# Kernel tuning notes

Measured on AMD Instinct MI355X. Metric: run time of the kernel, lower is better.

Reference implementation:

```python
import jax, jax.numpy as jnp
import numpy as np

G = 8          # GroupNorm groups
EPS = 1e-5
L = 4          # num_layers
C = 64         # hidden_channels
CIN = 2        # in_channels


def group_norm(x, gamma, beta):
    B, Cc, H, W = x.shape
    xr = x.reshape(B, G, Cc // G, H, W)
    mu = xr.mean(axis=(2, 3, 4), keepdims=True)
    var = xr.var(axis=(2, 3, 4), keepdims=True)
    xn = ((xr - mu) * jax.lax.rsqrt(var + EPS)).reshape(B, Cc, H, W)
    return xn * gamma[:, None, None] + beta[:, None, None]


def conv1x1(x, w, b):
    # x: [B,Ci,H,W], w: [Co,Ci] -> [B,Co,H,W]
    return jnp.einsum('bchw,oc->bohw', x, w) + b[None, :, None, None]


def conv3x3(x, w, b):
    y = jax.lax.conv_general_dilated(x, w, (1, 1), 'SAME',
                                     dimension_numbers=('NCHW', 'OIHW', 'NCHW'))
    return y + b[None, :, None, None]


def setup_inputs() -> dict:
    key = jax.random.key(0)
    ks = jax.random.split(key, 20)
    s = 0.05
    inp = {
        'x': jax.random.normal(ks[0], (2, CIN, 256, 256), jnp.float32),
        'hidden': jnp.zeros((2, L, C, C), jnp.float32),
        'W_in': jax.random.normal(ks[1], (C, CIN, 3, 3), jnp.float32) * s,
        'b_in': jnp.zeros((C,), jnp.float32),
        'gamma': jnp.ones((L, C), jnp.float32),
        'beta': jnp.zeros((L, C), jnp.float32),
        'Wq': jax.random.normal(ks[2], (L, C, C), jnp.float32) * s,
        'bq': jnp.zeros((L, C), jnp.float32),
        'Wk': jax.random.normal(ks[3], (L, C, C), jnp.float32) * s,
        'bk': jnp.zeros((L, C), jnp.float32),
        'Wv': jax.random.normal(ks[4], (L, C, C), jnp.float32) * s,
        'bv': jnp.zeros((L, C), jnp.float32),
        'Wg': jax.random.normal(ks[5], (L, 2 * C, C), jnp.float32) * s,
        'bg': jnp.zeros((L, 2 * C), jnp.float32),
        'Wp': jax.random.normal(ks[6], (L, C, C), jnp.float32) * s,
        'bp': jnp.zeros((L, C), jnp.float32),
        'W_out': jax.random.normal(ks[7], (CIN, C, 3, 3), jnp.float32) * s,
        'b_out': jnp.zeros((CIN,), jnp.float32),
    }
    return inp


def gla_layer(feat, prev_mem, gamma, beta, Wq, bq, Wk, bk, Wv, bv, Wg, bg, Wp, bp):
    B, Cc, H, W = feat.shape
    N = H * W
    scale = Cc ** (-0.5)
    xn = group_norm(feat, gamma, beta)
    q = conv1x1(xn, Wq, bq).reshape(B, Cc, N) * scale
    k = conv1x1(xn, Wk, bk).reshape(B, Cc, N)
    v = conv1x1(xn, Wv, bv).reshape(B, Cc, N)
    gates = conv1x1(xn, Wg, bg).reshape(B, 2 * Cc, N)
    f_gate = jax.nn.sigmoid(gates[:, :Cc])
    i_gate = jax.nn.sigmoid(gates[:, Cc:])
    k_gated = k * i_gate
    new_knowledge = jnp.einsum('bcn,bdn->bcd', k_gated, v) / N  # [B,C,C]
    global_forget = f_gate.mean(axis=2)[:, :, None]              # [B,C,1]
    new_mem = global_forget * prev_mem + new_knowledge
    retrieved = jnp.einsum('bcn,bcd->bdn', q, new_mem).reshape(B, Cc, H, W)
    out = conv1x1(retrieved, Wp, bp) + feat
    return out, new_mem


def reference(x, hidden, W_in, b_in, gamma, beta, Wq, bq, Wk, bk, Wv, bv,
              Wg, bg, Wp, bp, W_out, b_out):
    feat = conv3x3(x, W_in, b_in)
    mems = []
    for i in range(L):
        feat, m = gla_layer(feat, hidden[:, i], gamma[i], beta[i],
                            Wq[i], bq[i], Wk[i], bk[i], Wv[i], bv[i],
                            Wg[i], bg[i], Wp[i], bp[i])
        mems.append(m)
    new_hidden = jnp.stack(mems, axis=1)  # [B,L,C,C]
    out = conv3x3(feat, W_out, b_out) + x
    return out, new_hidden
```

## Files before the change

kernel.cpp:

```cpp
#include <hip/hip_runtime.h>
#include <hip/hip_bf16.h>

typedef __hip_bfloat16 bf16;
typedef __attribute__((ext_vector_type(8))) short bf16x8;
typedef __attribute__((ext_vector_type(4))) short short4v;
typedef __attribute__((ext_vector_type(4))) float f32x4;

#define BATCH 2
#define CH 64
#define NPIX 65536
#define HDIM 256
#define NLAYER 4
#define NGRP 8

#define OFS_FEAT   0ull
#define OFS_KNOW   33554432ull
#define OFS_FSUM   33685504ull
#define OFS_SSUM   33701888ull
#define OFS_BEFF   33718272ull
#define OFS_MEFFB  33718784ull
#define OFS_WKB    33735168ull
#define OFS_WVB    33767936ull
#define OFS_WGB    33800704ull
#define OFS_WTOUT  33866240ull
#define OFS_WPB    33870848ull
#define OFS_WQTB   33903616ull
#define ZERO_BYTES 163840

__device__ __forceinline__ float sigmoidf_(float x){ return 1.0f/(1.0f+__expf(-x)); }

__device__ __forceinline__ short f2bs(float x){
  unsigned u = __float_as_uint(x);
  u += 0x7fffu + ((u >> 16) & 1u);
  return (short)(u >> 16);
}

__device__ __forceinline__ float waveReduce(float v){
  #pragma unroll
  for (int off=32; off; off>>=1) v += __shfl_xor(v, off, 64);
  return v;
}

__global__ void k_prepw(const float* __restrict__ Wk, const float* __restrict__ Wv,
                        const float* __restrict__ Wg, const float* __restrict__ Wout,
                        const float* __restrict__ Wp, const float* __restrict__ Wq,
                        short* __restrict__ Wkb, short* __restrict__ Wvb,
                        short* __restrict__ Wgb, float* __restrict__ wtout,
                        short* __restrict__ Wpb, short* __restrict__ Wqtb){
  int i = blockIdx.x*256 + threadIdx.x;
  if (i < 16384){
    Wkb[i] = f2bs(Wk[i]);
    Wvb[i] = f2bs(Wv[i]);
    Wpb[i] = f2bs(Wp[i]);
    int l = i >> 12, within = i & 4095;
    int e = within >> 6, c = within & 63;
    Wqtb[i] = f2bs(Wq[l*4096 + c*64 + e]);
  }
  if (i < 32768) Wgb[i] = f2bs(Wg[i]);
  if (i < 1152){
    int o = i / 576, rem = i % 576;
    int k = rem >> 6, c = rem & 63;
    wtout[(o*9 + k)*64 + c] = Wout[o*576 + c*9 + k];
  }
}

__device__ __forceinline__ void blockStats(const float* gs, const float* gq,
                                           float* ssum_b, int t){
  __shared__ float sacc[16];
  if (t < 16) sacc[t] = 0.f;
  __syncthreads();
  #pragma unroll
  for (int g=0; g<NGRP; g++){
    float s  = waveReduce(gs[g]);
    float sq = waveReduce(gq[g]);
    if ((t & 63) == 0){ atomicAdd(&sacc[g*2], s); atomicAdd(&sacc[g*2+1], sq); }
  }
  __syncthreads();
  if (t < 16) atomicAdd(&ssum_b[t*32], sacc[t]);
}

__global__ void k_conv_in(const float* __restrict__ x, const float* __restrict__ w,
                          const float* __restrict__ bias,
                          float* __restrict__ feat, float* __restrict__ ssum){
  int b = blockIdx.y;
  int t = threadIdx.x;
  int n = blockIdx.x*256 + t;
  int y = n >> 8, xx = n & 255;
  float patch[18];
  int idx = 0;
  #pragma unroll
  for (int ci=0; ci<2; ci++)
    #pragma unroll
    for (int dy=-1; dy<=1; dy++)
      #pragma unroll
      for (int dx=-1; dx<=1; dx++){
        int yy = y+dy, xc = xx+dx;
        float v = 0.f;
        if (yy>=0 && yy<HDIM && xc>=0 && xc<HDIM)
          v = x[((b*2+ci)*HDIM + yy)*HDIM + xc];
        patch[idx++] = v;
      }
  float gs[NGRP], gq[NGRP];
  #pragma unroll
  for (int g=0; g<NGRP; g++){ gs[g]=0.f; gq[g]=0.f; }
  float* fb = feat + ((size_t)b*NPIX + n)*64;
  #pragma unroll
  for (int c4=0; c4<16; c4++){
    f32x4 ov;
    #pragma unroll
    for (int j=0;j<4;j++){
      int o = c4*4 + j;
      float acc = bias[o];
      #pragma unroll
      for (int k=0; k<18; k++) acc += w[o*18+k]*patch[k];
      ov[j] = acc;
      gs[o>>3] += acc; gq[o>>3] += acc*acc;
    }
    *(f32x4*)(fb + c4*4) = ov;
  }
  blockStats(gs, gq, ssum + b*512, t);
}

__device__ __forceinline__ void gnCoef(const float* __restrict__ ssum_l, int b, int t,
                                       const float* __restrict__ gammaP,
                                       const float* __restrict__ betaP, int l,
                                       float* s_gnA, float* s_gnB){
  if (t < 64){
    int g = t >> 3;
    const float inv = 1.0f/(8.0f*NPIX);
    float s  = ssum_l[(b*16 + g*2)*32];
    float sq = ssum_l[(b*16 + g*2 + 1)*32];
    float mu = s*inv;
    float var = sq*inv - mu*mu;
    float rstd = rsqrtf(var + 1e-5f);
    float A = rstd * gammaP[l*64 + t];
    s_gnA[t] = A;
    s_gnB[t] = betaP[l*64 + t] - mu * A;
  }
}

__global__ __launch_bounds__(256,3) void k_qkvg_know(
    const float* __restrict__ feat, const float* __restrict__ ssum_l,
    const float* __restrict__ gammaP, const float* __restrict__ betaP,
    const short* __restrict__ Wkb, const float* __restrict__ bkP,
    const short* __restrict__ Wvb, const float* __restrict__ bvP,
    const short* __restrict__ Wgb, const float* __restrict__ bgP,
    int l, float* __restrict__ know, float* __restrict__ f_sum)
{
  int b = blockIdx.y;
  int n0 = blockIdx.x * 128;
  int rep = blockIdx.x & 3;
  int t = threadIdx.x;
  int w = t >> 6;
  int lane = t & 63;
  int m = lane & 15;
  int quad = lane >> 4;
  int rowbase = w*16;

  __shared__ short s_buf[17408];
  short* s_kg = s_buf;
  short* s_v  = s_buf + 8704;
  short* s_xn = s_buf;
  __shared__ float s_gnA[64], s_gnB[64];

  gnCoef(ssum_l, b, t, gammaP, betaP, l, s_gnA, s_gnB);

  float bkv[4], biv[4], bvv[4], bfv[4], fs[4];
  #pragma unroll
  for (int r=0;r<4;r++){
    int row = rowbase + quad*4 + r;
    bkv[r] = bkP[l*64 + row];
    biv[r] = bgP[l*128 + 64 + row];
    bvv[r] = bvP[l*64 + row];
    bfv[r] = bgP[l*128 + row];
    fs[r] = 0.f;
  }
  f32x4 z4 = {0.f,0.f,0.f,0.f};
  f32x4 accn[4];
  #pragma unroll
  for (int dt=0;dt<4;dt++) accn[dt] = z4;

  __syncthreads();

  const float* fbase = feat + ((size_t)b*NPIX + n0)*64;
  #pragma unroll
  for (int i=0;i<8;i++){
    int chunk = t + i*256;
    int px = chunk >> 4, cq = chunk & 15;
    f32x4 fv = *(const f32x4*)(fbase + px*64 + cq*4);
    short4v xs;
    #pragma unroll
    for (int j=0;j<4;j++)
      xs[j] = f2bs(fmaf(fv[j], s_gnA[cq*4+j], s_gnB[cq*4+j]));
    *(short4v*)&s_xn[px*72 + cq*4] = xs;
  }
  __syncthreads();

  bf16x8 Bf[2][8];
  #pragma unroll
  for (int kc=0;kc<2;kc++)
    #pragma unroll
    for (int nt=0;nt<8;nt++)
      Bf[kc][nt] = *(const bf16x8*)&s_xn[(nt*16+m)*72 + kc*32 + quad*8];
  __syncthreads();

  {
    bf16x8 Ak[2], Ai[2];
    #pragma unroll
    for (int kc=0;kc<2;kc++){
      Ak[kc] = *(const bf16x8*)&Wkb[l*4096 + (rowbase+m)*64 + kc*32 + quad*8];
      Ai[kc] = *(const bf16x8*)&Wgb[l*8192 + (64+rowbase+m)*64 + kc*32 + quad*8];
    }
    #pragma unroll
    for (int half=0; half<2; half++){
      f32x4 acck[4], acci[4];
      #pragma unroll
      for (int q4=0;q4<4;q4++){ acck[q4]=z4; acci[q4]=z4; }
      #pragma unroll
      for (int kc=0;kc<2;kc++)
        #pragma unroll
        for (int q4=0;q4<4;q4++){
          acck[q4] = __builtin_amdgcn_mfma_f32_16x16x32_bf16(Ak[kc], Bf[kc][half*4+q4], acck[q4], 0,0,0);
          acci[q4] = __builtin_amdgcn_mfma_f32_16x16x32_bf16(Ai[kc], Bf[kc][half*4+q4], acci[q4], 0,0,0);
        }
      #pragma unroll
      for (int q4=0;q4<4;q4++){
        int nt = half*4+q4;
        #pragma unroll
        for (int r=0;r<4;r++){
          int row = rowbase + quad*4 + r;
          float kv = acck[q4][r] + bkv[r];
          float iv = acci[q4][r] + biv[r];
          s_kg[row*136 + nt*16 + m] = f2bs(kv * sigmoidf_(iv));
        }
      }
    }
  }
  {
    bf16x8 Av[2];
    #pragma unroll
    for (int kc=0;kc<2;kc++)
      Av[kc] = *(const bf16x8*)&Wvb[l*4096 + (rowbase+m)*64 + kc*32 + quad*8];
    #pragma unroll
    for (int half=0; half<2; half++){
      f32x4 accv[4];
      #pragma unroll
      for (int q4=0;q4<4;q4++) accv[q4]=z4;
      #pragma unroll
      for (int kc=0;kc<2;kc++)
        #pragma unroll
        for (int q4=0;q4<4;q4++)
          accv[q4] = __builtin_amdgcn_mfma_f32_16x16x32_bf16(Av[kc], Bf[kc][half*4+q4], accv[q4], 0,0,0);
      #pragma unroll
      for (int q4=0;q4<4;q4++){
        int nt = half*4+q4;
        #pragma unroll
        for (int r=0;r<4;r++){
          int row = rowbase + quad*4 + r;
          s_v[row*136 + nt*16 + m] = f2bs(accv[q4][r] + bvv[r]);
        }
      }
    }
  }
  {
    bf16x8 Af[2];
    #pragma unroll
    for (int kc=0;kc<2;kc++)
      Af[kc] = *(const bf16x8*)&Wgb[l*8192 + (rowbase+m)*64 + kc*32 + quad*8];
    #pragma unroll
    for (int half=0; half<2; half++){
      f32x4 accf[4];
      #pragma unroll
      for (int q4=0;q4<4;q4++) accf[q4]=z4;
      #pragma unroll
      for (int kc=0;kc<2;kc++)
        #pragma unroll
        for (int q4=0;q4<4;q4++)
          accf[q4] = __builtin_amdgcn_mfma_f32_16x16x32_bf16(Af[kc], Bf[kc][half*4+q4], accf[q4], 0,0,0);
      #pragma unroll
      for (int q4=0;q4<4;q4++)
        #pragma unroll
        for (int r=0;r<4;r++)
          fs[r] += sigmoidf_(accf[q4][r] + bfv[r]);
    }
  }
  __syncthreads();

  #pragma unroll
  for (int kc4=0; kc4<4; kc4++){
    bf16x8 a = *(const bf16x8*)&s_kg[(rowbase + m)*136 + kc4*32 + quad*8];
    #pragma unroll
    for (int dt=0; dt<4; dt++){
      bf16x8 bv8 = *(const bf16x8*)&s_v[(dt*16 + m)*136 + kc4*32 + quad*8];
      accn[dt] = __builtin_amdgcn_mfma_f32_16x16x32_bf16(a, bv8, accn[dt], 0,0,0);
    }
  }

  #pragma unroll
  for (int off=1; off<16; off<<=1)
    #pragma unroll
    for (int r=0;r<4;r++) fs[r] += __shfl_xor(fs[r], off, 64);
  if (m == 0){
    #pragma unroll
    for (int r=0;r<4;r++)
      atomicAdd(&f_sum[(b*64 + rowbase + quad*4 + r)*32], fs[r]);
  }
  float* kr = know + (size_t)(rep*2 + b)*4096;
  #pragma unroll
  for (int dt=0;dt<4;dt++)
    #pragma unroll
    for (int r=0;r<4;r++)
      atomicAdd(&kr[(rowbase + quad*4 + r)*64 + dt*16 + m], accn[dt][r]);
}

__global__ __launch_bounds__(256) void k_memupd_meff(
    float* __restrict__ know, float* __restrict__ f_sum,
    const float* __restrict__ hidden_in,
    const short* __restrict__ Wpb, const short* __restrict__ Wqtb,
    const float* __restrict__ bqP, const float* __restrict__ bpP,
    int l, float* __restrict__ hidden_out,
    short* __restrict__ Meffb, float* __restrict__ beff,
    float* __restrict__ ssum_next)
{
  int b = blockIdx.x;
  int t = threadIdx.x;
  int w = t >> 6;
  int lane = t & 63;
  int m = lane & 15;
  int quad = lane >> 4;

  __shared__ short s_memb[64*72];
  __shared__ short s_mfb[64*72];
  __shared__ float s_bq[64];

  if (t < 64) s_bq[t] = bqP[l*64 + t];

  const float invN = 1.0f/(float)NPIX;
  #pragma unroll
  for (int i=0;i<16;i++){
    int cd = t + i*256;
    int c = cd >> 6, d = cd & 63;
    float fmean = f_sum[(b*64 + c)*32] * invN;
    float kn = 0.f;
    #pragma unroll
    for (int rep=0; rep<4; rep++){
      kn += know[(size_t)(rep*2+b)*4096 + cd];
      know[(size_t)(rep*2+b)*4096 + cd] = 0.f;
    }
    kn *= invN;
    float pm = hidden_in[(size_t)(b*NLAYER+l)*4096 + cd];
    float nm = fmean*pm + kn;
    hidden_out[(size_t)(b*NLAYER+l)*4096 + cd] = nm;
    s_memb[c*72 + d] = f2bs(nm);
  }
  __syncthreads();
  if (t < 64) f_sum[(b*64 + t)*32] = 0.f;
  if (t < 16) ssum_next[(b*16 + t)*32] = 0.f;

  f32x4 z4 = {0.f,0.f,0.f,0.f};

  bf16x8 Ap[2];
  #pragma unroll
  for (int kc=0;kc<2;kc++)
    Ap[kc] = *(const bf16x8*)&Wpb[l*4096 + (w*16+m)*64 + kc*32 + quad*8];

  float be[4];
  #pragma unroll
  for (int r=0;r<4;r++) be[r] = 0.f;

  #pragma unroll
  for (int ct=0; ct<4; ct++){
    f32x4 a = z4;
    #pragma unroll
    for (int kc=0;kc<2;kc++){
      bf16x8 Bm = *(const bf16x8*)&s_memb[(ct*16+m)*72 + kc*32 + quad*8];
      a = __builtin_amdgcn_mfma_f32_16x16x32_bf16(Ap[kc], Bm, a, 0,0,0);
    }
    int c = ct*16 + m;
    #pragma unroll
    for (int r=0;r<4;r++){
      int o = w*16 + quad*4 + r;
      s_mfb[o*72 + c] = f2bs(a[r]);
      be[r] += a[r] * s_bq[c];
    }
  }
  #pragma unroll
  for (int off=1; off<16; off<<=1)
    #pragma unroll
    for (int r=0;r<4;r++) be[r] += __shfl_xor(be[r], off, 64);
  if (m == 0){
    #pragma unroll
    for (int r=0;r<4;r++){
      int o = w*16 + quad*4 + r;
      beff[b*64 + o] = bpP[l*64 + o] + 0.125f*be[r];
    }
  }
  __syncthreads();

  bf16x8 Am2[2];
  #pragma unroll
  for (int kc=0;kc<2;kc++)
    Am2[kc] = *(const bf16x8*)&s_mfb[(w*16+m)*72 + kc*32 + quad*8];
  #pragma unroll
  for (int et=0; et<4; et++){
    f32x4 a = z4;
    #pragma unroll
    for (int kc=0;kc<2;kc++){
      bf16x8 Bq = *(const bf16x8*)&Wqtb[l*4096 + (et*16+m)*64 + kc*32 + quad*8];
      a = __builtin_amdgcn_mfma_f32_16x16x32_bf16(Am2[kc], Bq, a, 0,0,0);
    }
    #pragma unroll
    for (int r=0;r<4;r++){
      int o = w*16 + quad*4 + r;
      Meffb[(size_t)b*4096 + o*64 + et*16 + m] = f2bs(0.125f*a[r]);
    }
  }
}

__global__ __launch_bounds__(256,3) void k_retrproj(
    const float* __restrict__ ssum_l,
    const float* __restrict__ gammaP, const float* __restrict__ betaP,
    const short* __restrict__ Meffb, const float* __restrict__ beff,
    int l, float* __restrict__ feat, float* __restrict__ ssum_next)
{
  int b = blockIdx.y;
  int n0 = blockIdx.x * 128;
  int t = threadIdx.x;
  int w = t >> 6;
  int lane = t & 63;
  int m = lane & 15;
  int quad = lane >> 4;

  __shared__ float s_out[128*68];
  short* s_xn = (short*)s_out;
  __shared__ float s_gnA[64], s_gnB[64], s_beff[64];
  __shared__ float s_sacc[16];

  gnCoef(ssum_l, b, t, gammaP, betaP, l, s_gnA, s_gnB);
  if (t < 64) s_beff[t] = beff[b*64 + t];
  if (t < 16) s_sacc[t] = 0.f;
  __syncthreads();

  const float* fbase = feat + ((size_t)b*NPIX + n0)*64;
  #pragma unroll
  for (int i=0;i<8;i++){
    int chunk = t + i*256;
    int px = chunk >> 4, cq = chunk & 15;
    f32x4 fv = *(const f32x4*)(fbase + px*64 + cq*4);
    short4v xs;
    #pragma unroll
    for (int j=0;j<4;j++)
      xs[j] = f2bs(fmaf(fv[j], s_gnA[cq*4+j], s_gnB[cq*4+j]));
    *(short4v*)&s_xn[px*72 + cq*4] = xs;
  }
  __syncthreads();

  bf16x8 Bf[2][8];
  #pragma unroll
  for (int kc=0;kc<2;kc++)
    #pragma unroll
    for (int nt=0;nt<8;nt++)
      Bf[kc][nt] = *(const bf16x8*)&s_xn[(nt*16+m)*72 + kc*32 + quad*8];

  bf16x8 Am[2];
  #pragma unroll
  for (int kc=0;kc<2;kc++)
    Am[kc] = *(const bf16x8*)&Meffb[(size_t)b*4096 + (w*16 + m)*64 + kc*32 + quad*8];
  __syncthreads();

  f32x4 acc[8];
  f32x4 z4 = {0.f,0.f,0.f,0.f};
  #pragma unroll
  for (int nt=0;nt<8;nt++) acc[nt]=z4;
  #pragma unroll
  for (int kc=0;kc<2;kc++)
    #pragma unroll
    for (int nt=0;nt<8;nt++)
      acc[nt] = __builtin_amdgcn_mfma_f32_16x16x32_bf16(Am[kc], Bf[kc][nt], acc[nt], 0,0,0);

  #pragma unroll
  for (int nt=0;nt<8;nt++)
    #pragma unroll
    for (int r=0;r<4;r++)
      s_out[(nt*16+m)*68 + w*16 + quad*4 + r] = acc[nt][r];
  __syncthreads();

  float gsv = 0.f, gqv = 0.f;
  int cq = t & 15;
  #pragma unroll
  for (int i=0;i<8;i++){
    int chunk = t + i*256;
    int px = chunk >> 4;
    float* fp = (float*)(fbase + px*64 + cq*4);
    f32x4 fv = *(const f32x4*)fp;
    f32x4 ov = *(const f32x4*)&s_out[px*68 + cq*4];
    f32x4 res;
    #pragma unroll
    for (int j=0;j<4;j++){
      float o = fv[j] + ov[j] + s_beff[cq*4+j];
      res[j] = o;
      gsv += o; gqv += o*o;
    }
    *(f32x4*)fp = res;
  }
  gsv += __shfl_xor(gsv, 1, 64);  gqv += __shfl_xor(gqv, 1, 64);
  gsv += __shfl_xor(gsv, 16, 64); gqv += __shfl_xor(gqv, 16, 64);
  gsv += __shfl_xor(gsv, 32, 64); gqv += __shfl_xor(gqv, 32, 64);
  if ((lane & 49) == 0){
    int g = (lane & 15) >> 1;
    atomicAdd(&s_sacc[g*2], gsv);
    atomicAdd(&s_sacc[g*2+1], gqv);
  }
  __syncthreads();
  if (t < 16) atomicAdd(&ssum_next[(b*16 + t)*32], s_sacc[t]);
}

__global__ void k_conv_out(const float* __restrict__ feat, const float* __restrict__ wt,
                           const float* __restrict__ bias,
                           const float* __restrict__ xin, float* __restrict__ out){
  int b = blockIdx.y;
  int y = blockIdx.x;
  int xx = threadIdx.x;
  float acc0 = bias[0], acc1 = bias[1];
  #pragma unroll
  for (int dy=-1; dy<=1; dy++){
    int yy = y + dy;
    if (yy < 0 || yy >= HDIM) continue;
    #pragma unroll
    for (int dx=-1; dx<=1; dx++){
      int xc = xx + dx;
      if (xc >= 0 && xc < HDIM){
        const float* fp = feat + ((size_t)b*NPIX + yy*HDIM + xc)*64;
        const float* w0 = wt + ((0*3 + dy+1)*3 + dx+1)*64;
        const float* w1 = wt + ((1*3 + dy+1)*3 + dx+1)*64;
        #pragma unroll
        for (int c4=0;c4<16;c4++){
          f32x4 fv  = *(const f32x4*)(fp + c4*4);
          f32x4 wv0 = *(const f32x4*)(w0 + c4*4);
          f32x4 wv1 = *(const f32x4*)(w1 + c4*4);
          #pragma unroll
          for (int j=0;j<4;j++){
            acc0 += fv[j]*wv0[j];
            acc1 += fv[j]*wv1[j];
          }
        }
      }
    }
  }
  size_t p0 = (size_t)(b*2+0)*NPIX + y*HDIM + xx;
  size_t p1 = (size_t)(b*2+1)*NPIX + y*HDIM + xx;
  out[p0] = acc0 + xin[p0];
  out[p1] = acc1 + xin[p1];
}

extern "C" void kernel_launch(void* const* d_in, const int* in_sizes, int n_in,
                              void* d_out, int out_size, void* d_ws, size_t ws_size,
                              hipStream_t stream){
  char* ws = (char*)d_ws;
  float* feat  = (float*)(ws + OFS_FEAT);
  float* know  = (float*)(ws + OFS_KNOW);
  float* fsum  = (float*)(ws + OFS_FSUM);
  float* ssum  = (float*)(ws + OFS_SSUM);
  float* beff  = (float*)(ws + OFS_BEFF);
  short* meffb = (short*)(ws + OFS_MEFFB);
  short* wkb   = (short*)(ws + OFS_WKB);
  short* wvb   = (short*)(ws + OFS_WVB);
  short* wgb   = (short*)(ws + OFS_WGB);
  float* wtout = (float*)(ws + OFS_WTOUT);
  short* wpb   = (short*)(ws + OFS_WPB);
  short* wqtb  = (short*)(ws + OFS_WQTB);

  const float* x      = (const float*)d_in[0];
  const float* hidden = (const float*)d_in[1];
  const float* W_in   = (const float*)d_in[2];
  const float* b_in   = (const float*)d_in[3];
  const float* gamma  = (const float*)d_in[4];
  const float* beta   = (const float*)d_in[5];
  const float* Wq     = (const float*)d_in[6];
  const float* bq     = (const float*)d_in[7];
  const float* Wk     = (const float*)d_in[8];
  const float* bk     = (const float*)d_in[9];
  const float* Wv     = (const float*)d_in[10];
  const float* bv     = (const float*)d_in[11];
  const float* Wg     = (const float*)d_in[12];
  const float* bg     = (const float*)d_in[13];
  const float* Wp     = (const float*)d_in[14];
  const float* bp     = (const float*)d_in[15];
  const float* W_out  = (const float*)d_in[16];
  const float* b_out  = (const float*)d_in[17];

  float* out        = (float*)d_out;
  float* hidden_out = out + BATCH*2*NPIX;

  hipMemsetAsync(ws + OFS_KNOW, 0, ZERO_BYTES, stream);
  k_prepw<<<dim3(128), dim3(256), 0, stream>>>(Wk, Wv, Wg, W_out, Wp, Wq,
                                               wkb, wvb, wgb, wtout, wpb, wqtb);
  k_conv_in<<<dim3(HDIM, BATCH), dim3(256), 0, stream>>>(x, W_in, b_in, feat, ssum);

  for (int l=0; l<NLAYER; l++){
    float* ssum_l = ssum + (l & 1)*1024;
    float* ssum_n = ssum + ((l+1) & 1)*1024;
    k_qkvg_know<<<dim3(NPIX/128, BATCH), dim3(256), 0, stream>>>(
        feat, ssum_l, gamma, beta, wkb, bk, wvb, bv, wgb, bg, l, know, fsum);
    k_memupd_meff<<<dim3(BATCH), dim3(256), 0, stream>>>(
        know, fsum, hidden, wpb, wqtb, bq, bp, l, hidden_out, meffb, beff, ssum_n);
    k_retrproj<<<dim3(NPIX/128, BATCH), dim3(256), 0, stream>>>(
        ssum_l, gamma, beta, meffb, beff, l, feat, ssum_n);
  }

  k_conv_out<<<dim3(HDIM, BATCH), dim3(256), 0, stream>>>(feat, wtout, b_out, x, out);
}
```

Baseline: 401.8 us.

## Fuse memory update into QKVG kernel via last-block counter; process two tiles per block

The separate per-layer memory-update kernel is removed. The last block to finish k_qkvg_know, detected with a global atomic counter and threadfences, now reduces the knowledge partials, updates the memory and builds the effective retrieval matrix. Both large kernels also loop over two 128-pixel tiles per block, halving the grid, which amortises setup work and the atomics on the knowledge partials. In exchange the tail block runs serial work at the end of the kernel, and the halved grid may lower occupancy or latency hiding.

```diff
diff --git a/kernel.cpp b/kernel.cpp
--- a/kernel.cpp
+++ b/kernel.cpp
@@ -17,15 +17,16 @@
 #define OFS_KNOW   33554432ull
 #define OFS_FSUM   33685504ull
 #define OFS_SSUM   33701888ull
-#define OFS_BEFF   33718272ull
-#define OFS_MEFFB  33718784ull
-#define OFS_WKB    33735168ull
-#define OFS_WVB    33767936ull
-#define OFS_WGB    33800704ull
-#define OFS_WTOUT  33866240ull
-#define OFS_WPB    33870848ull
-#define OFS_WQTB   33903616ull
-#define ZERO_BYTES 163840
+#define OFS_CNT    33718272ull
+#define OFS_BEFF   33718784ull
+#define OFS_MEFFB  33719296ull
+#define OFS_WKB    33735680ull
+#define OFS_WVB    33768448ull
+#define OFS_WGB    33801216ull
+#define OFS_WTOUT  33866752ull
+#define OFS_WPB    33871360ull
+#define OFS_WQTB   33904128ull
+#define ZERO_BYTES 164352
 
 __device__ __forceinline__ float sigmoidf_(float x){ return 1.0f/(1.0f+__expf(-x)); }
 
@@ -145,10 +146,15 @@
     const short* __restrict__ Wkb, const float* __restrict__ bkP,
     const short* __restrict__ Wvb, const float* __restrict__ bvP,
     const short* __restrict__ Wgb, const float* __restrict__ bgP,
-    int l, float* __restrict__ know, float* __restrict__ f_sum)
+    int l, float* __restrict__ know, float* __restrict__ f_sum,
+    const float* __restrict__ hidden_in,
+    const short* __restrict__ Wpb, const short* __restrict__ Wqtb,
+    const float* __restrict__ bqP, const float* __restrict__ bpP,
+    float* __restrict__ hidden_out,
+    short* __restrict__ Meffb, float* __restrict__ beff,
+    float* __restrict__ ssum_next, unsigned* __restrict__ cnt)
 {
   int b = blockIdx.y;
-  int n0 = blockIdx.x * 128;
   int rep = blockIdx.x & 3;
   int t = threadIdx.x;
   int w = t >> 6;
@@ -162,6 +168,7 @@
   short* s_v  = s_buf + 8704;
   short* s_xn = s_buf;
   __shared__ float s_gnA[64], s_gnB[64];
+  __shared__ unsigned s_done;
 
   gnCoef(ssum_l, b, t, gammaP, betaP, l, s_gnA, s_gnB);
 
@@ -182,118 +189,123 @@
 
   __syncthreads();
 
-  const float* fbase = feat + ((size_t)b*NPIX + n0)*64;
-  #pragma unroll
-  for (int i=0;i<8;i++){
-    int chunk = t + i*256;
-    int px = chunk >> 4, cq = chunk & 15;
-    f32x4 fv = *(const f32x4*)(fbase + px*64 + cq*4);
-    short4v xs;
-    #pragma unroll
-    for (int j=0;j<4;j++)
-      xs[j] = f2bs(fmaf(fv[j], s_gnA[cq*4+j], s_gnB[cq*4+j]));
-    *(short4v*)&s_xn[px*72 + cq*4] = xs;
-  }
-  __syncthreads();
-
-  bf16x8 Bf[2][8];
-  #pragma unroll
-  for (int kc=0;kc<2;kc++)
-    #pragma unroll
-    for (int nt=0;nt<8;nt++)
-      Bf[kc][nt] = *(const bf16x8*)&s_xn[(nt*16+m)*72 + kc*32 + quad*8];
-  __syncthreads();
-
-  {
-    bf16x8 Ak[2], Ai[2];
-    #pragma unroll
-    for (int kc=0;kc<2;kc++){
-      Ak[kc] = *(const bf16x8*)&Wkb[l*4096 + (rowbase+m)*64 + kc*32 + quad*8];
-      Ai[kc] = *(const bf16x8*)&Wgb[l*8192 + (64+rowbase+m)*64 + kc*32 + quad*8];
-    }
-    #pragma unroll
-    for (int half=0; half<2; half++){
-      f32x4 acck[4], acci[4];
-      #pragma unroll
-      for (int q4=0;q4<4;q4++){ acck[q4]=z4; acci[q4]=z4; }
+  for (int h=0; h<2; h++){
+    int n0 = blockIdx.x * 256 + h*128;
+    const float* fbase = feat + ((size_t)b*NPIX + n0)*64;
+
+    #pragma unroll
+    for (int i=0;i<8;i++){
+      int chunk = t + i*256;
+      int px = chunk >> 4, cq = chunk & 15;
+      f32x4 fv = *(const f32x4*)(fbase + px*64 + cq*4);
+      short4v xs;
+      #pragma unroll
+      for (int j=0;j<4;j++)
+        xs[j] = f2bs(fmaf(fv[j], s_gnA[cq*4+j], s_gnB[cq*4+j]));
+      *(short4v*)&s_xn[px*72 + cq*4] = xs;
+    }
+    __syncthreads();
+
+    bf16x8 Bf[2][8];
+    #pragma unroll
+    for (int kc=0;kc<2;kc++)
+      #pragma unroll
+      for (int nt=0;nt<8;nt++)
+        Bf[kc][nt] = *(const bf16x8*)&s_xn[(nt*16+m)*72 + kc*32 + quad*8];
+    __syncthreads();
+
+    {
+      bf16x8 Ak[2], Ai[2];
+      #pragma unroll
+      for (int kc=0;kc<2;kc++){
+        Ak[kc] = *(const bf16x8*)&Wkb[l*4096 + (rowbase+m)*64 + kc*32 + quad*8];
+        Ai[kc] = *(const bf16x8*)&Wgb[l*8192 + (64+rowbase+m)*64 + kc*32 + quad*8];
+      }
+      #pragma unroll
+      for (int half=0; half<2; half++){
+        f32x4 acck[4], acci[4];
+        #pragma unroll
+        for (int q4=0;q4<4;q4++){ acck[q4]=z4; acci[q4]=z4; }
+        #pragma unroll
+        for (int kc=0;kc<2;kc++)
+          #pragma unroll
+          for (int q4=0;q4<4;q4++){
+            acck[q4] = __builtin_amdgcn_mfma_f32_16x16x32_bf16(Ak[kc], Bf[kc][half*4+q4], acck[q4], 0,0,0);
+            acci[q4] = __builtin_amdgcn_mfma_f32_16x16x32_bf16(Ai[kc], Bf[kc][half*4+q4], acci[q4], 0,0,0);
+          }
+        #pragma unroll
+        for (int q4=0;q4<4;q4++){
+          int nt = half*4+q4;
+          #pragma unroll
+          for (int r=0;r<4;r++){
+            int row = rowbase + quad*4 + r;
+            float kv = acck[q4][r] + bkv[r];
+            float iv = acci[q4][r] + biv[r];
+            s_kg[row*136 + nt*16 + m] = f2bs(kv * sigmoidf_(iv));
+          }
+        }
+      }
+    }
+    {
+      bf16x8 Av[2];
       #pragma unroll
       for (int kc=0;kc<2;kc++)
+        Av[kc] = *(const bf16x8*)&Wvb[l*4096 + (rowbase+m)*64 + kc*32 + quad*8];
+      #pragma unroll
+      for (int half=0; half<2; half++){
+        f32x4 accv[4];
+        #pragma unroll
+        for (int q4=0;q4<4;q4++) accv[q4]=z4;
+        #pragma unroll
+        for (int kc=0;kc<2;kc++)
+          #pragma unroll
+          for (int q4=0;q4<4;q4++)
+            accv[q4] = __builtin_amdgcn_mfma_f32_16x16x32_bf16(Av[kc], Bf[kc][half*4+q4], accv[q4], 0,0,0);
         #pragma unroll
         for (int q4=0;q4<4;q4++){
-          acck[q4] = __builtin_amdgcn_mfma_f32_16x16x32_bf16(Ak[kc], Bf[kc][half*4+q4], acck[q4], 0,0,0);
-          acci[q4] = __builtin_amdgcn_mfma_f32_16x16x32_bf16(Ai[kc], Bf[kc][half*4+q4], acci[q4], 0,0,0);
+          int nt = half*4+q4;
+          #pragma unroll
+          for (int r=0;r<4;r++){
+            int row = rowbase + quad*4 + r;
+            s_v[row*136 + nt*16 + m] = f2bs(accv[q4][r] + bvv[r]);
+          }
         }
-      #pragma unroll
-      for (int q4=0;q4<4;q4++){
-        int nt = half*4+q4;
-        #pragma unroll
-        for (int r=0;r<4;r++){
-          int row = rowbase + quad*4 + r;
-          float kv = acck[q4][r] + bkv[r];
-          float iv = acci[q4][r] + biv[r];
-          s_kg[row*136 + nt*16 + m] = f2bs(kv * sigmoidf_(iv));
-        }
-      }
-    }
-  }
-  {
-    bf16x8 Av[2];
-    #pragma unroll
-    for (int kc=0;kc<2;kc++)
-      Av[kc] = *(const bf16x8*)&Wvb[l*4096 + (rowbase+m)*64 + kc*32 + quad*8];
-    #pragma unroll
-    for (int half=0; half<2; half++){
-      f32x4 accv[4];
-      #pragma unroll
-      for (int q4=0;q4<4;q4++) accv[q4]=z4;
+      }
+    }
+    {
+      bf16x8 Af[2];
       #pragma unroll
       for (int kc=0;kc<2;kc++)
+        Af[kc] = *(const bf16x8*)&Wgb[l*8192 + (rowbase+m)*64 + kc*32 + quad*8];
+      #pragma unroll
+      for (int half=0; half<2; half++){
+        f32x4 accf[4];
+        #pragma unroll
+        for (int q4=0;q4<4;q4++) accf[q4]=z4;
+        #pragma unroll
+        for (int kc=0;kc<2;kc++)
+          #pragma unroll
+          for (int q4=0;q4<4;q4++)
+            accf[q4] = __builtin_amdgcn_mfma_f32_16x16x32_bf16(Af[kc], Bf[kc][half*4+q4], accf[q4], 0,0,0);
         #pragma unroll
         for (int q4=0;q4<4;q4++)
-          accv[q4] = __builtin_amdgcn_mfma_f32_16x16x32_bf16(Av[kc], Bf[kc][half*4+q4], accv[q4], 0,0,0);
-      #pragma unroll
-      for (int q4=0;q4<4;q4++){
-        int nt = half*4+q4;
-        #pragma unroll
-        for (int r=0;r<4;r++){
-          int row = rowbase + quad*4 + r;
-          s_v[row*136 + nt*16 + m] = f2bs(accv[q4][r] + bvv[r]);
-        }
-      }
-    }
-  }
-  {
-    bf16x8 Af[2];
-    #pragma unroll
-    for (int kc=0;kc<2;kc++)
-      Af[kc] = *(const bf16x8*)&Wgb[l*8192 + (rowbase+m)*64 + kc*32 + quad*8];
-    #pragma unroll
-    for (int half=0; half<2; half++){
-      f32x4 accf[4];
-      #pragma unroll
-      for (int q4=0;q4<4;q4++) accf[q4]=z4;
-      #pragma unroll
-      for (int kc=0;kc<2;kc++)
-        #pragma unroll
-        for (int q4=0;q4<4;q4++)
-          accf[q4] = __builtin_amdgcn_mfma_f32_16x16x32_bf16(Af[kc], Bf[kc][half*4+q4], accf[q4], 0,0,0);
-      #pragma unroll
-      for (int q4=0;q4<4;q4++)
-        #pragma unroll
-        for (int r=0;r<4;r++)
-          fs[r] += sigmoidf_(accf[q4][r] + bfv[r]);
-    }
-  }
-  __syncthreads();
-
-  #pragma unroll
-  for (int kc4=0; kc4<4; kc4++){
-    bf16x8 a = *(const bf16x8*)&s_kg[(rowbase + m)*136 + kc4*32 + quad*8];
-    #pragma unroll
-    for (int dt=0; dt<4; dt++){
-      bf16x8 bv8 = *(const bf16x8*)&s_v[(dt*16 + m)*136 + kc4*32 + quad*8];
-      accn[dt] = __builtin_amdgcn_mfma_f32_16x16x32_bf16(a, bv8, accn[dt], 0,0,0);
-    }
+          #pragma unroll
+          for (int r=0;r<4;r++)
+            fs[r] += sigmoidf_(accf[q4][r] + bfv[r]);
+      }
+    }
+    __syncthreads();
+
+    #pragma unroll
+    for (int kc4=0; kc4<4; kc4++){
+      bf16x8 a = *(const bf16x8*)&s_kg[(rowbase + m)*136 + kc4*32 + quad*8];
+      #pragma unroll
+      for (int dt=0; dt<4; dt++){
+        bf16x8 bv8 = *(const bf16x8*)&s_v[(dt*16 + m)*136 + kc4*32 + quad*8];
+        accn[dt] = __builtin_amdgcn_mfma_f32_16x16x32_bf16(a, bv8, accn[dt], 0,0,0);
+      }
+    }
+    __syncthreads();
   }
 
   #pragma unroll
@@ -311,53 +323,38 @@
     #pragma unroll
     for (int r=0;r<4;r++)
       atomicAdd(&kr[(rowbase + quad*4 + r)*64 + dt*16 + m], accn[dt][r]);
-}
-
-__global__ __launch_bounds__(256) void k_memupd_meff(
-    float* __restrict__ know, float* __restrict__ f_sum,
-    const float* __restrict__ hidden_in,
-    const short* __restrict__ Wpb, const short* __restrict__ Wqtb,
-    const float* __restrict__ bqP, const float* __restrict__ bpP,
-    int l, float* __restrict__ hidden_out,
-    short* __restrict__ Meffb, float* __restrict__ beff,
-    float* __restrict__ ssum_next)
-{
-  int b = blockIdx.x;
-  int t = threadIdx.x;
-  int w = t >> 6;
-  int lane = t & 63;
-  int m = lane & 15;
-  int quad = lane >> 4;
-
-  __shared__ short s_memb[64*72];
-  __shared__ short s_mfb[64*72];
-  __shared__ float s_bq[64];
-
-  if (t < 64) s_bq[t] = bqP[l*64 + t];
-
+
+  __threadfence();
+  if (t == 0) s_done = atomicAdd(&cnt[l*2 + b], 1u);
+  __syncthreads();
+  if (s_done != gridDim.x - 1) return;
+  __threadfence();
+
+  short* s_memb = s_buf;
+  short* s_mfb  = s_buf + 4608;
   const float invN = 1.0f/(float)NPIX;
+
+  if (t < 64){
+    s_gnA[t] = atomicExch(&f_sum[(b*64 + t)*32], 0.f) * invN;
+    s_gnB[t] = bqP[l*64 + t];
+  }
+  if (t < 16) ssum_next[(b*16 + t)*32] = 0.f;
+  __syncthreads();
+
   #pragma unroll
   for (int i=0;i<16;i++){
     int cd = t + i*256;
     int c = cd >> 6, d = cd & 63;
-    float fmean = f_sum[(b*64 + c)*32] * invN;
     float kn = 0.f;
     #pragma unroll
-    for (int rep=0; rep<4; rep++){
-      kn += know[(size_t)(rep*2+b)*4096 + cd];
-      know[(size_t)(rep*2+b)*4096 + cd] = 0.f;
-    }
-    kn *= invN;
+    for (int rp=0; rp<4; rp++)
+      kn += atomicExch(&know[(size_t)(rp*2+b)*4096 + cd], 0.f);
     float pm = hidden_in[(size_t)(b*NLAYER+l)*4096 + cd];
-    float nm = fmean*pm + kn;
+    float nm = s_gnA[c]*pm + kn*invN;
     hidden_out[(size_t)(b*NLAYER+l)*4096 + cd] = nm;
     s_memb[c*72 + d] = f2bs(nm);
   }
   __syncthreads();
-  if (t < 64) f_sum[(b*64 + t)*32] = 0.f;
-  if (t < 16) ssum_next[(b*16 + t)*32] = 0.f;
-
-  f32x4 z4 = {0.f,0.f,0.f,0.f};
 
   bf16x8 Ap[2];
   #pragma unroll
@@ -381,7 +378,7 @@
     for (int r=0;r<4;r++){
       int o = w*16 + quad*4 + r;
       s_mfb[o*72 + c] = f2bs(a[r]);
-      be[r] += a[r] * s_bq[c];
+      be[r] += a[r] * s_gnB[c];
     }
   }
   #pragma unroll
@@ -424,7 +421,6 @@
     int l, float* __restrict__ feat, float* __restrict__ ssum_next)
 {
   int b = blockIdx.y;
-  int n0 = blockIdx.x * 128;
   int t = threadIdx.x;
   int w = t >> 6;
   int lane = t & 63;
@@ -439,70 +435,78 @@
   gnCoef(ssum_l, b, t, gammaP, betaP, l, s_gnA, s_gnB);
   if (t < 64) s_beff[t] = beff[b*64 + t];
   if (t < 16) s_sacc[t] = 0.f;
-  __syncthreads();
-
-  const float* fbase = feat + ((size_t)b*NPIX + n0)*64;
-  #pragma unroll
-  for (int i=0;i<8;i++){
-    int chunk = t + i*256;
-    int px = chunk >> 4, cq = chunk & 15;
-    f32x4 fv = *(const f32x4*)(fbase + px*64 + cq*4);
-    short4v xs;
-    #pragma unroll
-    for (int j=0;j<4;j++)
-      xs[j] = f2bs(fmaf(fv[j], s_gnA[cq*4+j], s_gnB[cq*4+j]));
-    *(short4v*)&s_xn[px*72 + cq*4] = xs;
-  }
-  __syncthreads();
-
-  bf16x8 Bf[2][8];
-  #pragma unroll
-  for (int kc=0;kc<2;kc++)
-    #pragma unroll
-    for (int nt=0;nt<8;nt++)
-      Bf[kc][nt] = *(const bf16x8*)&s_xn[(nt*16+m)*72 + kc*32 + quad*8];
 
   bf16x8 Am[2];
   #pragma unroll
   for (int kc=0;kc<2;kc++)
     Am[kc] = *(const bf16x8*)&Meffb[(size_t)b*4096 + (w*16 + m)*64 + kc*32 + quad*8];
-  __syncthreads();
-
-  f32x4 acc[8];
-  f32x4 z4 = {0.f,0.f,0.f,0.f};
-  #pragma unroll
-  for (int nt=0;nt<8;nt++) acc[nt]=z4;
-  #pragma unroll
-  for (int kc=0;kc<2;kc++)
-    #pragma unroll
-    for (int nt=0;nt<8;nt++)
-      acc[nt] = __builtin_amdgcn_mfma_f32_16x16x32_bf16(Am[kc], Bf[kc][nt], acc[nt], 0,0,0);
-
-  #pragma unroll
-  for (int nt=0;nt<8;nt++)
-    #pragma unroll
-    for (int r=0;r<4;r++)
-      s_out[(nt*16+m)*68 + w*16 + quad*4 + r] = acc[nt][r];
+
   __syncthreads();
 
   float gsv = 0.f, gqv = 0.f;
   int cq = t & 15;
-  #pragma unroll
-  for (int i=0;i<8;i++){
-    int chunk = t + i*256;
-    int px = chunk >> 4;
-    float* fp = (float*)(fbase + px*64 + cq*4);
-    f32x4 fv = *(const f32x4*)fp;
-    f32x4 ov = *(const f32x4*)&s_out[px*68 + cq*4];
-    f32x4 res;
-    #pragma unroll
-    for (int j=0;j<4;j++){
-      float o = fv[j] + ov[j] + s_beff[cq*4+j];
-      res[j] = o;
-      gsv += o; gqv += o*o;
-    }
-    *(f32x4*)fp = res;
-  }
+
+  for (int h=0; h<2; h++){
+    int n0 = blockIdx.x * 256 + h*128;
+    const float* fbase = feat + ((size_t)b*NPIX + n0)*64;
+
+    #pragma unroll
+    for (int i=0;i<8;i++){
+      int chunk = t + i*256;
+      int px = chunk >> 4, cqi = chunk & 15;
+      f32x4 fv = *(const f32x4*)(fbase + px*64 + cqi*4);
+      short4v xs;
+      #pragma unroll
+      for (int j=0;j<4;j++)
+        xs[j] = f2bs(fmaf(fv[j], s_gnA[cqi*4+j], s_gnB[cqi*4+j]));
+      *(short4v*)&s_xn[px*72 + cqi*4] = xs;
+    }
+    __syncthreads();
+
+    bf16x8 Bf[2][8];
+    #pragma unroll
+    for (int kc=0;kc<2;kc++)
+      #pragma unroll
+      for (int nt=0;nt<8;nt++)
+        Bf[kc][nt] = *(const bf16x8*)&s_xn[(nt*16+m)*72 + kc*32 + quad*8];
+    __syncthreads();
+
+    f32x4 acc[8];
+    f32x4 z4 = {0.f,0.f,0.f,0.f};
+    #pragma unroll
+    for (int nt=0;nt<8;nt++) acc[nt]=z4;
+    #pragma unroll
+    for (int kc=0;kc<2;kc++)
+      #pragma unroll
+      for (int nt=0;nt<8;nt++)
+        acc[nt] = __builtin_amdgcn_mfma_f32_16x16x32_bf16(Am[kc], Bf[kc][nt], acc[nt], 0,0,0);
+
+    #pragma unroll
+    for (int nt=0;nt<8;nt++)
+      #pragma unroll
+      for (int r=0;r<4;r++)
+        s_out[(nt*16+m)*68 + w*16 + quad*4 + r] = acc[nt][r];
+    __syncthreads();
+
+    #pragma unroll
+    for (int i=0;i<8;i++){
+      int chunk = t + i*256;
+      int px = chunk >> 4;
+      float* fp = (float*)(fbase + px*64 + cq*4);
+      f32x4 fv = *(const f32x4*)fp;
+      f32x4 ov = *(const f32x4*)&s_out[px*68 + cq*4];
+      f32x4 res;
+      #pragma unroll
+      for (int j=0;j<4;j++){
+        float o = fv[j] + ov[j] + s_beff[cq*4+j];
+        res[j] = o;
+        gsv += o; gqv += o*o;
+      }
+      *(f32x4*)fp = res;
+    }
+    __syncthreads();
+  }
+
   gsv += __shfl_xor(gsv, 1, 64);  gqv += __shfl_xor(gqv, 1, 64);
   gsv += __shfl_xor(gsv, 16, 64); gqv += __shfl_xor(gqv, 16, 64);
   gsv += __shfl_xor(gsv, 32, 64); gqv += __shfl_xor(gqv, 32, 64);
@@ -561,6 +565,7 @@
   float* know  = (float*)(ws + OFS_KNOW);
   float* fsum  = (float*)(ws + OFS_FSUM);
   float* ssum  = (float*)(ws + OFS_SSUM);
+  unsigned* cnt = (unsigned*)(ws + OFS_CNT);
   float* beff  = (float*)(ws + OFS_BEFF);
   short* meffb = (short*)(ws + OFS_MEFFB);
   short* wkb   = (short*)(ws + OFS_WKB);
@@ -600,11 +605,10 @@
   for (int l=0; l<NLAYER; l++){
     float* ssum_l = ssum + (l & 1)*1024;
     float* ssum_n = ssum + ((l+1) & 1)*1024;
-    k_qkvg_know<<<dim3(NPIX/128, BATCH), dim3(256), 0, stream>>>(
-        feat, ssum_l, gamma, beta, wkb, bk, wvb, bv, wgb, bg, l, know, fsum);
-    k_memupd_meff<<<dim3(BATCH), dim3(256), 0, stream>>>(
-        know, fsum, hidden, wpb, wqtb, bq, bp, l, hidden_out, meffb, beff, ssum_n);
-    k_retrproj<<<dim3(NPIX/128, BATCH), dim3(256), 0, stream>>>(
+    k_qkvg_know<<<dim3(NPIX/256, BATCH), dim3(256), 0, stream>>>(
+        feat, ssum_l, gamma, beta, wkb, bk, wvb, bv, wgb, bg, l, know, fsum,
+        hidden, wpb, wqtb, bq, bp, hidden_out, meffb, beff, ssum_n, cnt);
+    k_retrproj<<<dim3(NPIX/256, BATCH), dim3(256), 0, stream>>>(
         ssum_l, gamma, beta, meffb, beff, l, feat, ssum_n);
   }
 
```

Measured after the change: 599.6 us. 1.49x slower.

## Replace atomic knowledge accumulation with per-block slots and a separate reduction kernel

Applied to the files above, without the earlier changes.

Each qkvg block now writes its 64x64 partial k·v product to its own slot with plain stores, where it previously did float atomicAdds into four replicated buffers. A new k_memreduce kernel sums the 512 slots per batch across 64 blocks and computes the new memory, and the old single-kernel memory update is split into reduce and Meff stages. The aim is to remove contention on the atomics. In exchange it adds 16 MB of slot writes and reads per layer plus one more kernel launch.

```diff
diff --git a/kernel.cpp b/kernel.cpp
--- a/kernel.cpp
+++ b/kernel.cpp
@@ -12,20 +12,22 @@
 #define HDIM 256
 #define NLAYER 4
 #define NGRP 8
+#define NSLOT 512
 
 #define OFS_FEAT   0ull
-#define OFS_KNOW   33554432ull
-#define OFS_FSUM   33685504ull
-#define OFS_SSUM   33701888ull
-#define OFS_BEFF   33718272ull
-#define OFS_MEFFB  33718784ull
-#define OFS_WKB    33735168ull
-#define OFS_WVB    33767936ull
-#define OFS_WGB    33800704ull
-#define OFS_WTOUT  33866240ull
-#define OFS_WPB    33870848ull
-#define OFS_WQTB   33903616ull
-#define ZERO_BYTES 163840
+#define OFS_KSLOT  33554432ull
+#define OFS_MEMBG  50331648ull
+#define OFS_FSUM   50348032ull
+#define OFS_SSUM   50364416ull
+#define OFS_BEFF   50380800ull
+#define OFS_MEFFB  50381312ull
+#define OFS_WKB    50397696ull
+#define OFS_WVB    50430464ull
+#define OFS_WGB    50463232ull
+#define OFS_WTOUT  50528768ull
+#define OFS_WPB    50533376ull
+#define OFS_WQTB   50566144ull
+#define ZERO_BYTES 32768
 
 __device__ __forceinline__ float sigmoidf_(float x){ return 1.0f/(1.0f+__expf(-x)); }
 
@@ -145,11 +147,10 @@
     const short* __restrict__ Wkb, const float* __restrict__ bkP,
     const short* __restrict__ Wvb, const float* __restrict__ bvP,
     const short* __restrict__ Wgb, const float* __restrict__ bgP,
-    int l, float* __restrict__ know, float* __restrict__ f_sum)
+    int l, float* __restrict__ kslot, float* __restrict__ f_sum)
 {
   int b = blockIdx.y;
   int n0 = blockIdx.x * 128;
-  int rep = blockIdx.x & 3;
   int t = threadIdx.x;
   int w = t >> 6;
   int lane = t & 63;
@@ -305,21 +306,49 @@
     for (int r=0;r<4;r++)
       atomicAdd(&f_sum[(b*64 + rowbase + quad*4 + r)*32], fs[r]);
   }
-  float* kr = know + (size_t)(rep*2 + b)*4096;
+  float* kr = kslot + ((size_t)b*NSLOT + blockIdx.x)*4096;
   #pragma unroll
   for (int dt=0;dt<4;dt++)
     #pragma unroll
     for (int r=0;r<4;r++)
-      atomicAdd(&kr[(rowbase + quad*4 + r)*64 + dt*16 + m], accn[dt][r]);
-}
-
-__global__ __launch_bounds__(256) void k_memupd_meff(
-    float* __restrict__ know, float* __restrict__ f_sum,
-    const float* __restrict__ hidden_in,
+      kr[(rowbase + quad*4 + r)*64 + dt*16 + m] = accn[dt][r];
+}
+
+__global__ __launch_bounds__(256) void k_memreduce(
+    const float* __restrict__ kslot, const float* __restrict__ f_sum,
+    const float* __restrict__ hidden_in, int l,
+    float* __restrict__ hidden_out, short* __restrict__ membG)
+{
+  int b = blockIdx.y;
+  int t = threadIdx.x;
+  int e = t & 127;
+  int half = t >> 7;
+  int cd = blockIdx.x*128 + e;
+
+  const float* base = kslot + ((size_t)b*NSLOT + half*256)*4096 + cd;
+  float s = 0.f;
+  #pragma unroll 16
+  for (int sl=0; sl<256; sl++) s += base[(size_t)sl*4096];
+
+  __shared__ float red[128];
+  if (half) red[e] = s;
+  __syncthreads();
+  if (!half){
+    const float invN = 1.0f/(float)NPIX;
+    float kn = (s + red[e]) * invN;
+    float fmean = f_sum[(b*64 + (cd>>6))*32] * invN;
+    float pm = hidden_in[(size_t)(b*NLAYER+l)*4096 + cd];
+    float nm = fmean*pm + kn;
+    hidden_out[(size_t)(b*NLAYER+l)*4096 + cd] = nm;
+    membG[b*4096 + cd] = f2bs(nm);
+  }
+}
+
+__global__ __launch_bounds__(256) void k_meff(
+    const short* __restrict__ membG, float* __restrict__ f_sum,
     const short* __restrict__ Wpb, const short* __restrict__ Wqtb,
     const float* __restrict__ bqP, const float* __restrict__ bpP,
-    int l, float* __restrict__ hidden_out,
-    short* __restrict__ Meffb, float* __restrict__ beff,
+    int l, short* __restrict__ Meffb, float* __restrict__ beff,
     float* __restrict__ ssum_next)
 {
   int b = blockIdx.x;
@@ -335,23 +364,11 @@
 
   if (t < 64) s_bq[t] = bqP[l*64 + t];
 
-  const float invN = 1.0f/(float)NPIX;
   #pragma unroll
   for (int i=0;i<16;i++){
     int cd = t + i*256;
     int c = cd >> 6, d = cd & 63;
-    float fmean = f_sum[(b*64 + c)*32] * invN;
-    float kn = 0.f;
-    #pragma unroll
-    for (int rep=0; rep<4; rep++){
-      kn += know[(size_t)(rep*2+b)*4096 + cd];
-      know[(size_t)(rep*2+b)*4096 + cd] = 0.f;
-    }
-    kn *= invN;
-    float pm = hidden_in[(size_t)(b*NLAYER+l)*4096 + cd];
-    float nm = fmean*pm + kn;
-    hidden_out[(size_t)(b*NLAYER+l)*4096 + cd] = nm;
-    s_memb[c*72 + d] = f2bs(nm);
+    s_memb[c*72 + d] = membG[b*4096 + cd];
   }
   __syncthreads();
   if (t < 64) f_sum[(b*64 + t)*32] = 0.f;
@@ -558,7 +575,8 @@
                               hipStream_t stream){
   char* ws = (char*)d_ws;
   float* feat  = (float*)(ws + OFS_FEAT);
-  float* know  = (float*)(ws + OFS_KNOW);
+  float* kslot = (float*)(ws + OFS_KSLOT);
+  short* membg = (short*)(ws + OFS_MEMBG);
   float* fsum  = (float*)(ws + OFS_FSUM);
   float* ssum  = (float*)(ws + OFS_SSUM);
   float* beff  = (float*)(ws + OFS_BEFF);
@@ -592,7 +610,7 @@
   float* out        = (float*)d_out;
   float* hidden_out = out + BATCH*2*NPIX;
 
-  hipMemsetAsync(ws + OFS_KNOW, 0, ZERO_BYTES, stream);
+  hipMemsetAsync(ws + OFS_FSUM, 0, ZERO_BYTES, stream);
   k_prepw<<<dim3(128), dim3(256), 0, stream>>>(Wk, Wv, Wg, W_out, Wp, Wq,
                                                wkb, wvb, wgb, wtout, wpb, wqtb);
   k_conv_in<<<dim3(HDIM, BATCH), dim3(256), 0, stream>>>(x, W_in, b_in, feat, ssum);
@@ -601,9 +619,11 @@
     float* ssum_l = ssum + (l & 1)*1024;
     float* ssum_n = ssum + ((l+1) & 1)*1024;
     k_qkvg_know<<<dim3(NPIX/128, BATCH), dim3(256), 0, stream>>>(
-        feat, ssum_l, gamma, beta, wkb, bk, wvb, bv, wgb, bg, l, know, fsum);
-    k_memupd_meff<<<dim3(BATCH), dim3(256), 0, stream>>>(
-        know, fsum, hidden, wpb, wqtb, bq, bp, l, hidden_out, meffb, beff, ssum_n);
+        feat, ssum_l, gamma, beta, wkb, bk, wvb, bv, wgb, bg, l, kslot, fsum);
+    k_memreduce<<<dim3(32, BATCH), dim3(256), 0, stream>>>(
+        kslot, fsum, hidden, l, hidden_out, membg);
+    k_meff<<<dim3(BATCH), dim3(256), 0, stream>>>(
+        membg, fsum, wpb, wqtb, bq, bp, l, meffb, beff, ssum_n);
     k_retrproj<<<dim3(NPIX/128, BATCH), dim3(256), 0, stream>>>(
         ssum_l, gamma, beta, meffb, beff, l, feat, ssum_n);
   }
```

Result: faster. 393.0 us (-2.2%).
